# Kernel optimization log

Hardware: AMD Instinct MI355X
Metric: run time of the kernel (lower is better)

## Reference

```python
import jax, jax.numpy as jnp
import numpy as np

FRAME_NUMBER = 1200

def _relgcn(x, W, rows, cols, vals, n_nodes):
    # Multi-relation sparse GCN: sum_r A_r @ (x @ W_r), then tanh.
    out = jnp.zeros((n_nodes, W.shape[-1]), dtype=x.dtype)
    for r in range(W.shape[0]):  # fixed small set of relations (5)
        xl = x @ W[r]                              # [N, D]
        msgs = vals[r][:, None] * xl[cols[r]]      # [E, D] gather
        out = out + jax.ops.segment_sum(msgs, rows[r], num_segments=n_nodes)
    return jnp.tanh(out)

def setup_inputs() -> dict:
    key = jax.random.key(0)
    ks = jax.random.split(key, 20)
    N, E, R, D, B, C = 11201, 100000, 5, 512, 32, 16
    s = lambda k, sh, sc=0.05: jax.random.normal(k, sh, dtype=jnp.float32) * sc
    return {
        "target_span": jax.random.normal(ks[0], (B, 4 * 512), dtype=jnp.float32),
        "frame_emb": s(ks[1], (FRAME_NUMBER + 1, D), 1.0),
        "role_emb": s(ks[2], (10001, D), 1.0),
        "rel_W0": s(ks[3], (R, D, D)),
        "rel_W1": s(ks[4], (R, D, D)),
        "span_W1": s(ks[5], (2048, 2048)),
        "span_b1": s(ks[6], (2048,)),
        "span_W2": s(ks[7], (2048, D)),
        "span_b2": s(ks[8], (D,)),
        "fp_W1": s(ks[9], (D, D)),
        "fp_b1": s(ks[10], (D,)),
        "fp_W2": s(ks[11], (D, D)),
        "fp_b2": s(ks[12], (D,)),
        "adj_vals": jax.random.uniform(ks[13], (R, E), dtype=jnp.float32),
        "fe_ids": jax.random.randint(ks[14], (10001,), 0, 10001),
        "adj_rows": jax.random.randint(ks[15], (R, E), 0, N),
        "adj_cols": jax.random.randint(ks[16], (R, E), 0, N),
        "gold_frame_id": jax.random.randint(ks[17], (B,), 0, C),
        "frame_list": jax.random.randint(ks[18], (B, C), 0, FRAME_NUMBER),
    }

def reference(target_span, frame_emb, role_emb, rel_W0, rel_W1,
              span_W1, span_b1, span_W2, span_b2,
              fp_W1, fp_b1, fp_W2, fp_b2, adj_vals,
              fe_ids, adj_rows, adj_cols, gold_frame_id, frame_list):
    B = target_span.shape[0]
    # Embedding lookups (frame_embedding(arange(frame_number)), role_embedding(fe_dict ids))
    all_frame = frame_emb[:FRAME_NUMBER]            # [1200, D]
    all_fe = role_emb[fe_ids]                       # [10001, D]
    x = jnp.concatenate([all_frame, all_fe], axis=0)  # [N, D]
    N = x.shape[0]
    # Two-layer multi-relation GCN over 5 sparse adjacencies
    x = _relgcn(x, rel_W0, adj_rows, adj_cols, adj_vals, N)
    all_embeddings = _relgcn(x, rel_W1, adj_rows, adj_cols, adj_vals, N)  # [N, D]
    # span_fc_layer Mlp: Linear(2048,2048) -> ReLU -> Linear(2048,512) (dropout in eval = identity)
    target_node = jax.nn.relu(target_span @ span_W1 + span_b1) @ span_W2 + span_b2  # [B, D]
    # frame_pred = RoleClassification: Linear -> ReLU -> Linear -> Tanh, then bmm with all node embeddings
    Q = jnp.tanh(jax.nn.relu(target_node @ fp_W1 + fp_b1) @ fp_W2 + fp_b2)          # [B, D]
    pred_frame_weight = jnp.einsum("nd,bd->bn", all_embeddings, Q)[:, :FRAME_NUMBER]  # [B, 1200]
    # gold frame path: one-hot select gold frame id from candidates, gather its node embedding
    gold_frame_label = jnp.take_along_axis(frame_list, gold_frame_id[:, None], axis=1)[:, 0]  # [B]
    frame_node = all_embeddings[gold_frame_label]   # [B, D] (embed_dropout in eval = identity)
    return jnp.concatenate([pred_frame_weight, frame_node], axis=-1)  # [B, 1200+512]
```

## Files before the change

kernel.cpp:

```cpp
#include <hip/hip_runtime.h>
#include <hip/hip_bf16.h>
#include <stdint.h>

typedef unsigned short u16;
typedef __attribute__((ext_vector_type(8))) short short8;
typedef __attribute__((ext_vector_type(4))) float float4v;

#define NNODES 11201
#define MPAD   11264
#define EEDGES 100000
#define RREL   5
#define DDIM   512
#define XLW    2560
#define FRAMES 1200
#define OUTC   1712

__device__ __forceinline__ float bf2f(u16 h) {
    return __uint_as_float(((uint32_t)h) << 16);
}
__device__ __forceinline__ u16 f2bf(float f) {
    uint32_t x = __float_as_uint(f);
    x += 0x7fffu + ((x >> 16) & 1u);
    return (u16)(x >> 16);
}
__device__ __forceinline__ float fast_tanh(float v) {
    v = fminf(fmaxf(v, -10.f), 10.f);
    float ex = __expf(2.f * v);
    return (ex - 1.f) / (ex + 1.f);
}

__global__ void hist_k(const int* __restrict__ rows, int* __restrict__ counts) {
    int tid = blockIdx.x * 256 + threadIdx.x;
    if (tid >= RREL * EEDGES) return;
    int r = tid / EEDGES;
    atomicAdd(&counts[r * NNODES + rows[tid]], 1);
}

__global__ __launch_bounds__(1024) void scan_offsets(const int* __restrict__ counts,
                                                     int* __restrict__ offs,
                                                     int* __restrict__ cursor) {
    const int PER = 11;
    int r = blockIdx.x;
    const int* c = counts + (size_t)r * NNODES;
    int* o = offs + (size_t)r * (NNODES + 1);
    int* cur = cursor + (size_t)r * NNODES;
    __shared__ int wsum[16];
    const int lane = threadIdx.x & 63, wid = threadIdx.x >> 6;
    int base = threadIdx.x * PER;
    int v[PER];
    int s = 0;
    #pragma unroll
    for (int t = 0; t < PER; ++t) {
        int idx = base + t;
        v[t] = (idx < NNODES) ? c[idx] : 0;
        s += v[t];
    }
    int incl = s;
    #pragma unroll
    for (int d = 1; d < 64; d <<= 1) {
        int t = __shfl_up(incl, d, 64);
        if (lane >= d) incl += t;
    }
    if (lane == 63) wsum[wid] = incl;
    __syncthreads();
    if (wid == 0) {
        int wv = (lane < 16) ? wsum[lane] : 0;
        #pragma unroll
        for (int d = 1; d < 16; d <<= 1) {
            int t = __shfl_up(wv, d, 64);
            if (lane >= d) wv += t;
        }
        if (lane < 16) wsum[lane] = wv;
    }
    __syncthreads();
    int run = incl - s + ((wid > 0) ? wsum[wid - 1] : 0);
    #pragma unroll
    for (int t = 0; t < PER; ++t) {
        int idx = base + t;
        if (idx < NNODES) { o[idx] = run; cur[idx] = run; }
        run += v[t];
    }
    if (threadIdx.x == 1023) o[NNODES] = run;
}

__global__ void scatter_k(const int* __restrict__ rows, const int* __restrict__ cols,
                          const float* __restrict__ vals, int* __restrict__ cursor,
                          int* __restrict__ colS, float* __restrict__ valS) {
    int tid = blockIdx.x * 256 + threadIdx.x;
    if (tid >= RREL * EEDGES) return;
    int r = tid / EEDGES;
    int row = rows[tid];
    int pos = atomicAdd(&cursor[r * NNODES + row], 1);
    colS[(size_t)r * EEDGES + pos] = cols[tid];
    valS[(size_t)r * EEDGES + pos] = vals[tid];
}

#define BX_BLOCKS 5601
#define TSP_BLOCKS 256
#define TR_BASE (BX_BLOCKS + TSP_BLOCKS)
__global__ void prep_all(const float* __restrict__ frame_emb,
                         const float* __restrict__ role_emb,
                         const int* __restrict__ fe_ids,
                         const float* __restrict__ ts,
                         const float* __restrict__ w0, const float* __restrict__ w1,
                         const float* __restrict__ s1, const float* __restrict__ s2,
                         const float* __restrict__ f1, const float* __restrict__ f2,
                         u16* __restrict__ x, u16* __restrict__ tsp,
                         u16* __restrict__ w0t, u16* __restrict__ w1t,
                         u16* __restrict__ s1t, u16* __restrict__ s2t,
                         u16* __restrict__ f1t, u16* __restrict__ f2t) {
    int bid = blockIdx.x;
    if (bid < BX_BLOCKS) {
        int t = bid * 256 + threadIdx.x;
        int row = t >> 7, c4 = (t & 127) << 2;
        if (row >= NNODES) return;
        const float* src = (row < FRAMES) ? (frame_emb + (size_t)row * DDIM)
                                          : (role_emb + (size_t)fe_ids[row - FRAMES] * DDIM);
        float4 v = *(const float4*)(src + c4);
        ushort4 o = { f2bf(v.x), f2bf(v.y), f2bf(v.z), f2bf(v.w) };
        *(ushort4*)(x + (size_t)row * DDIM + c4) = o;
        return;
    }
    if (bid < TR_BASE) {
        int t = (bid - BX_BLOCKS) * 256 + threadIdx.x;
        int row = t >> 9, c4 = (t & 511) << 2;
        ushort4 o = {0, 0, 0, 0};
        if (row < 32) {
            float4 v = *(const float4*)(ts + (size_t)row * 2048 + c4);
            o = ushort4{ f2bf(v.x), f2bf(v.y), f2bf(v.z), f2bf(v.w) };
        }
        *(ushort4*)(tsp + (size_t)row * 2048 + c4) = o;
        return;
    }
    int b = bid - TR_BASE;
    const float* src; u16* dst;
    int cols, ldOut, bx, by;
    size_t zcol = 0;
    if (b < 1280) {
        int rel = b >> 8, rem = b & 255;
        src = w0 + (size_t)rel * 262144; dst = w0t;
        cols = 512; ldOut = XLW; zcol = (size_t)rel * 512;
        bx = rem & 15; by = rem >> 4;
    } else if (b < 2560) {
        b -= 1280;
        int rel = b >> 8, rem = b & 255;
        src = w1 + (size_t)rel * 262144; dst = w1t;
        cols = 512; ldOut = XLW; zcol = (size_t)rel * 512;
        bx = rem & 15; by = rem >> 4;
    } else if (b < 6656) {
        b -= 2560;
        src = s1; dst = s1t; cols = 2048; ldOut = 2048;
        bx = b & 63; by = b >> 6;
    } else if (b < 7680) {
        b -= 6656;
        src = s2; dst = s2t; cols = 512; ldOut = 2048;
        bx = b & 15; by = b >> 4;
    } else if (b < 7936) {
        b -= 7680;
        src = f1; dst = f1t; cols = 512; ldOut = 512;
        bx = b & 15; by = b >> 4;
    } else {
        b -= 7936;
        src = f2; dst = f2t; cols = 512; ldOut = 512;
        bx = b & 15; by = b >> 4;
    }
    __shared__ u16 tile[32][33];
    int c0 = bx * 32, r0 = by * 32;
    int tx = threadIdx.x & 31, ty = threadIdx.x >> 5;
    #pragma unroll
    for (int i = 0; i < 4; ++i) {
        int rr = ty + i * 8;
        tile[rr][tx] = f2bf(src[(size_t)(r0 + rr) * cols + c0 + tx]);
    }
    __syncthreads();
    #pragma unroll
    for (int i = 0; i < 4; ++i) {
        int rr = ty + i * 8;
        dst[(size_t)(c0 + rr) * ldOut + zcol + r0 + tx] = tile[tx][rr];
    }
}

template<int EPI, bool FOUT, bool GUARDS>
__global__ __launch_bounds__(256)
void gemm_n64(const u16* __restrict__ A, const u16* __restrict__ Bt,
              void* __restrict__ Cv, int K, int lda, int ldb, int ldc,
              int mGuard, int nGuard)
{
    __shared__ u16 As[2][128 * 32];
    __shared__ u16 Bs[2][64 * 32];
    const int tid = threadIdx.x;
    const int wave = tid >> 6, lane = tid & 63;
    const int m0 = blockIdx.x * 128, n0 = blockIdx.y * 64;
    const int srow = lane >> 2;
    const int skoff = (lane & 3) << 3;
    const int fr = lane & 15, quad = lane >> 4;
    const int wm = (wave & 1) << 6;
    const int wn = (wave >> 1) << 5;
    float4v acc[4][2] = {};

    const u16* Abase = A  + (size_t)(m0 + srow) * lda + skoff;
    const u16* Bbase = Bt + (size_t)(n0 + srow) * ldb + skoff;

    auto stage = [&](int buf, int k0) {
        #pragma unroll
        for (int i = 0; i < 2; ++i) {
            const int rb = (wave + i * 4) << 4;
            __builtin_amdgcn_global_load_lds(
                (const __attribute__((address_space(1))) unsigned int*)(Abase + (size_t)rb * lda + k0),
                (__attribute__((address_space(3))) unsigned int*)(&As[buf][rb * 32]), 16, 0, 0);
        }
        const int rbB = wave << 4;
        __builtin_amdgcn_global_load_lds(
            (const __attribute__((address_space(1))) unsigned int*)(Bbase + (size_t)rbB * ldb + k0),
            (__attribute__((address_space(3))) unsigned int*)(&Bs[buf][rbB * 32]), 16, 0, 0);
    };
    auto compute = [&](int buf) {
        short8 a[4], b[2];
        #pragma unroll
        for (int t = 0; t < 4; ++t)
            a[t] = *(const short8*)(&As[buf][((wm + t * 16 + fr) << 5) + (quad << 3)]);
        #pragma unroll
        for (int t = 0; t < 2; ++t)
            b[t] = *(const short8*)(&Bs[buf][((wn + t * 16 + fr) << 5) + (quad << 3)]);
        #pragma unroll
        for (int i = 0; i < 4; ++i)
            #pragma unroll
            for (int j = 0; j < 2; ++j)
                acc[i][j] = __builtin_amdgcn_mfma_f32_16x16x32_bf16(a[i], b[j], acc[i][j], 0, 0, 0);
    };

    stage(0, 0);
    __syncthreads();
    int cur = 0;
    for (int k0 = 32; k0 < K; k0 += 32) {
        stage(cur ^ 1, k0);
        compute(cur);
        __syncthreads();
        cur ^= 1;
    }
    compute(cur);

    #pragma unroll
    for (int i = 0; i < 4; ++i) {
        #pragma unroll
        for (int j = 0; j < 2; ++j) {
            const int n = n0 + wn + j * 16 + fr;
            #pragma unroll
            for (int rg = 0; rg < 4; ++rg) {
                const int m = m0 + wm + i * 16 + (quad << 2) + rg;
                if (GUARDS && (m >= mGuard || n >= nGuard)) continue;
                float v = acc[i][j][rg];
                if (EPI == 4) v = fast_tanh(v);
                if (FOUT) ((float*)Cv)[(size_t)m * ldc + n] = v;
                else      ((u16*)Cv)[(size_t)m * ldc + n] = f2bf(v);
            }
        }
    }
}

__global__ __launch_bounds__(256)
void gemm_sk(const u16* __restrict__ A, const u16* __restrict__ Bt,
             float* __restrict__ Cf, int Kc, int lda, int ldb, int ldc)
{
    __shared__ u16 As[2][128 * 32];
    __shared__ u16 Bs[2][128 * 32];
    const int tid = threadIdx.x;
    const int wave = tid >> 6, lane = tid & 63;
    const int m0 = blockIdx.y * 128, n0 = blockIdx.x * 128;
    const int kb = blockIdx.z * Kc;
    const int srow = lane >> 2;
    const int skoff = (lane & 3) << 3;
    const int fr = lane & 15, quad = lane >> 4;
    const int wm = (wave & 1) << 6, wn = (wave >> 1) << 6;
    float4v acc[4][4] = {};

    const u16* Abase = A  + (size_t)(m0 + srow) * lda + skoff;
    const u16* Bbase = Bt + (size_t)(n0 + srow) * ldb + skoff;

    auto stage = [&](int buf, int k0) {
        #pragma unroll
        for (int i = 0; i < 2; ++i) {
            const int rb = (wave + i * 4) << 4;
            __builtin_amdgcn_global_load_lds(
                (const __attribute__((address_space(1))) unsigned int*)(Abase + (size_t)rb * lda + k0),
                (__attribute__((address_space(3))) unsigned int*)(&As[buf][rb * 32]), 16, 0, 0);
            __builtin_amdgcn_global_load_lds(
                (const __attribute__((address_space(1))) unsigned int*)(Bbase + (size_t)rb * ldb + k0),
                (__attribute__((address_space(3))) unsigned int*)(&Bs[buf][rb * 32]), 16, 0, 0);
        }
    };
    auto compute = [&](int buf) {
        short8 a[4], b[4];
        #pragma unroll
        for (int t = 0; t < 4; ++t)
            a[t] = *(const short8*)(&As[buf][((wm + t * 16 + fr) << 5) + (quad << 3)]);
        #pragma unroll
        for (int t = 0; t < 4; ++t)
            b[t] = *(const short8*)(&Bs[buf][((wn + t * 16 + fr) << 5) + (quad << 3)]);
        #pragma unroll
        for (int i = 0; i < 4; ++i)
            #pragma unroll
            for (int j = 0; j < 4; ++j)
                acc[i][j] = __builtin_amdgcn_mfma_f32_16x16x32_bf16(a[i], b[j], acc[i][j], 0, 0, 0);
    };

    stage(0, kb);
    __syncthreads();
    int cur = 0;
    for (int k0 = kb + 32; k0 < kb + Kc; k0 += 32) {
        stage(cur ^ 1, k0);
        compute(cur);
        __syncthreads();
        cur ^= 1;
    }
    compute(cur);

    #pragma unroll
    for (int i = 0; i < 4; ++i)
        #pragma unroll
        for (int j = 0; j < 4; ++j) {
            const int n = n0 + wn + j * 16 + fr;
            #pragma unroll
            for (int rg = 0; rg < 4; ++rg) {
                const int m = m0 + wm + i * 16 + (quad << 2) + rg;
                atomicAdd(&Cf[(size_t)m * ldc + n], acc[i][j][rg]);
            }
        }
}

template<int ACT, bool HASB>
__global__ void sk_ep(const float* __restrict__ Cf, const float* __restrict__ bias,
                      u16* __restrict__ outp, int Ncols, int total4) {
    int t = blockIdx.x * 256 + threadIdx.x;
    if (t >= total4) return;
    int i = t << 2;
    float4 v = *(const float4*)(Cf + i);
    if (HASB) {
        int col = i & (Ncols - 1);
        v.x += bias[col]; v.y += bias[col + 1]; v.z += bias[col + 2]; v.w += bias[col + 3];
    }
    if (ACT == 1) { v.x = fmaxf(v.x, 0.f); v.y = fmaxf(v.y, 0.f);
                    v.z = fmaxf(v.z, 0.f); v.w = fmaxf(v.w, 0.f); }
    if (ACT == 3) { v.x = fast_tanh(v.x); v.y = fast_tanh(v.y);
                    v.z = fast_tanh(v.z); v.w = fast_tanh(v.w); }
    ushort4 o = { f2bf(v.x), f2bf(v.y), f2bf(v.z), f2bf(v.w) };
    *(ushort4*)(outp + i) = o;
}

__device__ __forceinline__ void fma8(float* acc, uint4 u, float val) {
    acc[0] = fmaf(val, __uint_as_float(u.x << 16), acc[0]);
    acc[1] = fmaf(val, __uint_as_float(u.x & 0xffff0000u), acc[1]);
    acc[2] = fmaf(val, __uint_as_float(u.y << 16), acc[2]);
    acc[3] = fmaf(val, __uint_as_float(u.y & 0xffff0000u), acc[3]);
    acc[4] = fmaf(val, __uint_as_float(u.z << 16), acc[4]);
    acc[5] = fmaf(val, __uint_as_float(u.z & 0xffff0000u), acc[5]);
    acc[6] = fmaf(val, __uint_as_float(u.w << 16), acc[6]);
    acc[7] = fmaf(val, __uint_as_float(u.w & 0xffff0000u), acc[7]);
}

__global__ __launch_bounds__(256)
void spmm_agg(const u16* __restrict__ x, const int* __restrict__ offs,
              const int* __restrict__ colS, const float* __restrict__ valS,
              u16* __restrict__ agg)
{
    const int wave = threadIdx.x >> 6, lane = threadIdx.x & 63;
    const int n = blockIdx.x * 4 + wave;
    const int r = blockIdx.y;
    if (n >= NNODES) return;
    const u16* xr = x + (lane << 3);
    int s = offs[r * (NNODES + 1) + n];
    const int e = offs[r * (NNODES + 1) + n + 1];
    const int*   cp = colS + (size_t)r * EEDGES;
    const float* vp = valS + (size_t)r * EEDGES;
    float acc[8] = {0.f, 0.f, 0.f, 0.f, 0.f, 0.f, 0.f, 0.f};
    while (s < e) {
        int m = e - s; if (m > 8) m = 8;
        int   ct[8]; float vt[8]; uint4 u[8];
        #pragma unroll
        for (int t = 0; t < 8; ++t)
            if (t < m) { ct[t] = cp[s + t]; vt[t] = vp[s + t]; }
        #pragma unroll
        for (int t = 0; t < 8; ++t)
            if (t < m) u[t] = *(const uint4*)(xr + (size_t)ct[t] * DDIM);
        #pragma unroll
        for (int t = 0; t < 8; ++t)
            if (t < m) fma8(acc, u[t], vt[t]);
        s += 8;
    }
    uint4 o;
    o.x = (uint32_t)f2bf(acc[0]) | ((uint32_t)f2bf(acc[1]) << 16);
    o.y = (uint32_t)f2bf(acc[2]) | ((uint32_t)f2bf(acc[3]) << 16);
    o.z = (uint32_t)f2bf(acc[4]) | ((uint32_t)f2bf(acc[5]) << 16);
    o.w = (uint32_t)f2bf(acc[6]) | ((uint32_t)f2bf(acc[7]) << 16);
    *(uint4*)(agg + (size_t)n * XLW + (r << 9) + (lane << 3)) = o;
}

__global__ void frame_gather(const u16* __restrict__ emb, const int* __restrict__ frame_list,
                             const int* __restrict__ gold, float* __restrict__ out) {
    int t = blockIdx.x * 256 + threadIdx.x;
    if (t >= 32 * 64) return;
    int b = t >> 6, lane = t & 63;
    int label = frame_list[b * 16 + gold[b]];
    const u16* src = emb + (size_t)label * DDIM + (lane << 3);
    float* dst = out + (size_t)b * OUTC + FRAMES + (lane << 3);
    float4 o0 = { bf2f(src[0]), bf2f(src[1]), bf2f(src[2]), bf2f(src[3]) };
    float4 o1 = { bf2f(src[4]), bf2f(src[5]), bf2f(src[6]), bf2f(src[7]) };
    *(float4*)(dst) = o0;
    *(float4*)(dst + 4) = o1;
}

extern "C" void kernel_launch(void* const* d_in, const int* in_sizes, int n_in,
                              void* d_out, int out_size, void* d_ws, size_t ws_size,
                              hipStream_t stream) {
    const float* target_span = (const float*)d_in[0];
    const float* frame_emb   = (const float*)d_in[1];
    const float* role_emb    = (const float*)d_in[2];
    const float* rel_W0      = (const float*)d_in[3];
    const float* rel_W1      = (const float*)d_in[4];
    const float* span_W1     = (const float*)d_in[5];
    const float* span_b1     = (const float*)d_in[6];
    const float* span_W2     = (const float*)d_in[7];
    const float* span_b2     = (const float*)d_in[8];
    const float* fp_W1       = (const float*)d_in[9];
    const float* fp_b1       = (const float*)d_in[10];
    const float* fp_W2       = (const float*)d_in[11];
    const float* fp_b2       = (const float*)d_in[12];
    const float* adj_vals    = (const float*)d_in[13];
    const int* fe_ids      = (const int*)d_in[14];
    const int* adj_rows    = (const int*)d_in[15];
    const int* adj_cols    = (const int*)d_in[16];
    const int* gold_id     = (const int*)d_in[17];
    const int* frame_list  = (const int*)d_in[18];
    float* out = (float*)d_out;

    char* ws = (char*)d_ws;
    size_t off = 0;
    auto take = [&](size_t bytes) -> char* {
        char* p = ws + off;
        off = (off + bytes + 255) & ~(size_t)255;
        return p;
    };
    u16* x      = (u16*)take((size_t)MPAD * DDIM * 2);
    u16* agg    = (u16*)take((size_t)MPAD * XLW * 2);
    u16* w0t    = (u16*)take((size_t)512 * XLW * 2);
    u16* w1t    = (u16*)take((size_t)512 * XLW * 2);
    u16* s1t    = (u16*)take((size_t)2048 * 2048 * 2);
    u16* s2t    = (u16*)take((size_t)512 * 2048 * 2);
    u16* f1t    = (u16*)take((size_t)512 * 512 * 2);
    u16* f2t    = (u16*)take((size_t)512 * 512 * 2);
    int* counts = (int*)take((size_t)RREL * NNODES * 4);
    int* offs   = (int*)take((size_t)RREL * (NNODES + 1) * 4);
    int* cursor = (int*)take((size_t)RREL * NNODES * 4);
    int* colS   = (int*)take((size_t)RREL * EEDGES * 4);
    float* valS = (float*)take((size_t)RREL * EEDGES * 4);
    u16* tsp    = (u16*)take((size_t)128 * 2048 * 2);
    u16* h1     = (u16*)take((size_t)128 * 2048 * 2);
    u16* tn     = (u16*)take((size_t)128 * 512 * 2);
    u16* h2     = (u16*)take((size_t)128 * 512 * 2);
    u16* Qb     = (u16*)take((size_t)128 * 512 * 2);
    float* CfAll = (float*)take((size_t)(128 * 2048 + 3 * 128 * 512) * 4);
    float* Cf1 = CfAll;
    float* Cf2 = Cf1 + 128 * 2048;
    float* Cf3 = Cf2 + 128 * 512;
    float* Cf4 = Cf3 + 128 * 512;

    hipMemsetAsync(counts, 0, (size_t)RREL * NNODES * 4, stream);
    hipMemsetAsync(CfAll, 0, (size_t)(128 * 2048 + 3 * 128 * 512) * 4, stream);

    hist_k<<<(RREL * EEDGES + 255) / 256, 256, 0, stream>>>(adj_rows, counts);
    scan_offsets<<<RREL, 1024, 0, stream>>>(counts, offs, cursor);
    scatter_k<<<(RREL * EEDGES + 255) / 256, 256, 0, stream>>>(adj_rows, adj_cols, adj_vals,
                                                               cursor, colS, valS);
    prep_all<<<TR_BASE + 8192, 256, 0, stream>>>(frame_emb, role_emb, fe_ids, target_span,
                                                 rel_W0, rel_W1, span_W1, span_W2, fp_W1, fp_W2,
                                                 x, tsp, w0t, w1t, s1t, s2t, f1t, f2t);

    spmm_agg<<<dim3((NNODES + 3) / 4, RREL), 256, 0, stream>>>(x, offs, colS, valS, agg);
    gemm_n64<4, false, true><<<dim3(MPAD / 128, 8), 256, 0, stream>>>(
        agg, w0t, x, XLW, XLW, XLW, 512, NNODES, 512);
    spmm_agg<<<dim3((NNODES + 3) / 4, RREL), 256, 0, stream>>>(x, offs, colS, valS, agg);
    gemm_n64<4, false, true><<<dim3(MPAD / 128, 8), 256, 0, stream>>>(
        agg, w1t, x, XLW, XLW, XLW, 512, NNODES, 512);

    gemm_sk<<<dim3(16, 1, 8), 256, 0, stream>>>(tsp, s1t, Cf1, 256, 2048, 2048, 2048);
    sk_ep<1, true><<<(128 * 2048 / 4 + 255) / 256, 256, 0, stream>>>(Cf1, span_b1, h1, 2048, 128 * 2048 / 4);
    gemm_sk<<<dim3(4, 1, 8), 256, 0, stream>>>(h1, s2t, Cf2, 256, 2048, 2048, 512);
    sk_ep<0, true><<<(128 * 512 / 4 + 255) / 256, 256, 0, stream>>>(Cf2, span_b2, tn, 512, 128 * 512 / 4);
    gemm_sk<<<dim3(4, 1, 4), 256, 0, stream>>>(tn, f1t, Cf3, 128, 512, 512, 512);
    sk_ep<1, true><<<(128 * 512 / 4 + 255) / 256, 256, 0, stream>>>(Cf3, fp_b1, h2, 512, 128 * 512 / 4);
    gemm_sk<<<dim3(4, 1, 4), 256, 0, stream>>>(h2, f2t, Cf4, 128, 512, 512, 512);
    sk_ep<3, true><<<(128 * 512 / 4 + 255) / 256, 256, 0, stream>>>(Cf4, fp_b2, Qb, 512, 128 * 512 / 4);

    gemm_n64<0, true, true><<<dim3(1, 19), 256, 0, stream>>>(
        Qb, x, out, 512, 512, 512, OUTC, 32, FRAMES);
    frame_gather<<<8, 256, 0, stream>>>(x, frame_list, gold_id, out);
}
```

Before: 485.9 us.

## Replace LDS-staged GEMM with direct register-load MFMA GEMM and merge memsets

The 128x64 tiled GEMM no longer stages A and B through double-buffered shared memory. Each wave now loads its MFMA fragments straight from global memory into registers and runs an unrolled K loop with no __syncthreads. This removes the LDS traffic and barrier overhead, but loses cross-wave reuse of the B tile: all four waves reload the same B rows and depend on cache hits. Separately, the workspace layout is reordered so one memset zeroes both the counts and split-K accumulator buffers, which also zeroes the buffers that lie between them.

Measured after the change: 707.6 us. 45.6% more time.

```diff
diff --git a/kernel.cpp b/kernel.cpp
--- a/kernel.cpp
+++ b/kernel.cpp
@@ -182,72 +182,45 @@
 
 template<int EPI, bool FOUT, bool GUARDS>
 __global__ __launch_bounds__(256)
-void gemm_n64(const u16* __restrict__ A, const u16* __restrict__ Bt,
+void gemm_reg(const u16* __restrict__ A, const u16* __restrict__ Bt,
               void* __restrict__ Cv, int K, int lda, int ldb, int ldc,
               int mGuard, int nGuard)
 {
-    __shared__ u16 As[2][128 * 32];
-    __shared__ u16 Bs[2][64 * 32];
-    const int tid = threadIdx.x;
-    const int wave = tid >> 6, lane = tid & 63;
+    const int lane = threadIdx.x & 63, wave = threadIdx.x >> 6;
+    const int fr = lane & 15, quad = lane >> 4;
     const int m0 = blockIdx.x * 128, n0 = blockIdx.y * 64;
-    const int srow = lane >> 2;
-    const int skoff = (lane & 3) << 3;
-    const int fr = lane & 15, quad = lane >> 4;
-    const int wm = (wave & 1) << 6;
-    const int wn = (wave >> 1) << 5;
-    float4v acc[4][2] = {};
-
-    const u16* Abase = A  + (size_t)(m0 + srow) * lda + skoff;
-    const u16* Bbase = Bt + (size_t)(n0 + srow) * ldb + skoff;
-
-    auto stage = [&](int buf, int k0) {
-        #pragma unroll
-        for (int i = 0; i < 2; ++i) {
-            const int rb = (wave + i * 4) << 4;
-            __builtin_amdgcn_global_load_lds(
-                (const __attribute__((address_space(1))) unsigned int*)(Abase + (size_t)rb * lda + k0),
-                (__attribute__((address_space(3))) unsigned int*)(&As[buf][rb * 32]), 16, 0, 0);
-        }
-        const int rbB = wave << 4;
-        __builtin_amdgcn_global_load_lds(
-            (const __attribute__((address_space(1))) unsigned int*)(Bbase + (size_t)rbB * ldb + k0),
-            (__attribute__((address_space(3))) unsigned int*)(&Bs[buf][rbB * 32]), 16, 0, 0);
-    };
-    auto compute = [&](int buf) {
-        short8 a[4], b[2];
-        #pragma unroll
-        for (int t = 0; t < 4; ++t)
-            a[t] = *(const short8*)(&As[buf][((wm + t * 16 + fr) << 5) + (quad << 3)]);
-        #pragma unroll
-        for (int t = 0; t < 2; ++t)
-            b[t] = *(const short8*)(&Bs[buf][((wn + t * 16 + fr) << 5) + (quad << 3)]);
-        #pragma unroll
-        for (int i = 0; i < 4; ++i)
-            #pragma unroll
-            for (int j = 0; j < 2; ++j)
-                acc[i][j] = __builtin_amdgcn_mfma_f32_16x16x32_bf16(a[i], b[j], acc[i][j], 0, 0, 0);
-    };
-
-    stage(0, 0);
-    __syncthreads();
-    int cur = 0;
-    for (int k0 = 32; k0 < K; k0 += 32) {
-        stage(cur ^ 1, k0);
-        compute(cur);
-        __syncthreads();
-        cur ^= 1;
-    }
-    compute(cur);
-
-    #pragma unroll
-    for (int i = 0; i < 4; ++i) {
-        #pragma unroll
-        for (int j = 0; j < 2; ++j) {
-            const int n = n0 + wn + j * 16 + fr;
+    const u16* Ap = A  + (size_t)(m0 + (wave << 5) + fr) * lda + (quad << 3);
+    const u16* Bp = Bt + (size_t)(n0 + fr) * ldb + (quad << 3);
+    const size_t lda16 = (size_t)lda * 16;
+    const size_t ldb16 = (size_t)ldb * 16;
+    float4v acc[2][4] = {};
+
+    #pragma unroll 4
+    for (int k0 = 0; k0 < K; k0 += 32) {
+        short8 a0 = *(const short8*)(Ap + k0);
+        short8 a1 = *(const short8*)(Ap + lda16 + k0);
+        short8 b0 = *(const short8*)(Bp + k0);
+        short8 b1 = *(const short8*)(Bp + ldb16 + k0);
+        short8 b2 = *(const short8*)(Bp + 2 * ldb16 + k0);
+        short8 b3 = *(const short8*)(Bp + 3 * ldb16 + k0);
+        acc[0][0] = __builtin_amdgcn_mfma_f32_16x16x32_bf16(a0, b0, acc[0][0], 0, 0, 0);
+        acc[0][1] = __builtin_amdgcn_mfma_f32_16x16x32_bf16(a0, b1, acc[0][1], 0, 0, 0);
+        acc[0][2] = __builtin_amdgcn_mfma_f32_16x16x32_bf16(a0, b2, acc[0][2], 0, 0, 0);
+        acc[0][3] = __builtin_amdgcn_mfma_f32_16x16x32_bf16(a0, b3, acc[0][3], 0, 0, 0);
+        acc[1][0] = __builtin_amdgcn_mfma_f32_16x16x32_bf16(a1, b0, acc[1][0], 0, 0, 0);
+        acc[1][1] = __builtin_amdgcn_mfma_f32_16x16x32_bf16(a1, b1, acc[1][1], 0, 0, 0);
+        acc[1][2] = __builtin_amdgcn_mfma_f32_16x16x32_bf16(a1, b2, acc[1][2], 0, 0, 0);
+        acc[1][3] = __builtin_amdgcn_mfma_f32_16x16x32_bf16(a1, b3, acc[1][3], 0, 0, 0);
+    }
+
+    #pragma unroll
+    for (int i = 0; i < 2; ++i) {
+        #pragma unroll
+        for (int j = 0; j < 4; ++j) {
+            const int n = n0 + j * 16 + fr;
             #pragma unroll
             for (int rg = 0; rg < 4; ++rg) {
-                const int m = m0 + wm + i * 16 + (quad << 2) + rg;
+                const int m = m0 + (wave << 5) + i * 16 + (quad << 2) + rg;
                 if (GUARDS && (m >= mGuard || n >= nGuard)) continue;
                 float v = acc[i][j][rg];
                 if (EPI == 4) v = fast_tanh(v);
@@ -449,6 +422,7 @@
     u16* f1t    = (u16*)take((size_t)512 * 512 * 2);
     u16* f2t    = (u16*)take((size_t)512 * 512 * 2);
     int* counts = (int*)take((size_t)RREL * NNODES * 4);
+    float* CfAll = (float*)take((size_t)(128 * 2048 + 3 * 128 * 512) * 4);
     int* offs   = (int*)take((size_t)RREL * (NNODES + 1) * 4);
     int* cursor = (int*)take((size_t)RREL * NNODES * 4);
     int* colS   = (int*)take((size_t)RREL * EEDGES * 4);
@@ -458,14 +432,13 @@
     u16* tn     = (u16*)take((size_t)128 * 512 * 2);
     u16* h2     = (u16*)take((size_t)128 * 512 * 2);
     u16* Qb     = (u16*)take((size_t)128 * 512 * 2);
-    float* CfAll = (float*)take((size_t)(128 * 2048 + 3 * 128 * 512) * 4);
     float* Cf1 = CfAll;
     float* Cf2 = Cf1 + 128 * 2048;
     float* Cf3 = Cf2 + 128 * 512;
     float* Cf4 = Cf3 + 128 * 512;
 
-    hipMemsetAsync(counts, 0, (size_t)RREL * NNODES * 4, stream);
-    hipMemsetAsync(CfAll, 0, (size_t)(128 * 2048 + 3 * 128 * 512) * 4, stream);
+    size_t zlen = (char*)(CfAll + 128 * 2048 + 3 * 128 * 512) - (char*)counts;
+    hipMemsetAsync(counts, 0, zlen, stream);
 
     hist_k<<<(RREL * EEDGES + 255) / 256, 256, 0, stream>>>(adj_rows, counts);
     scan_offsets<<<RREL, 1024, 0, stream>>>(counts, offs, cursor);
@@ -476,10 +449,10 @@
                                                  x, tsp, w0t, w1t, s1t, s2t, f1t, f2t);
 
     spmm_agg<<<dim3((NNODES + 3) / 4, RREL), 256, 0, stream>>>(x, offs, colS, valS, agg);
-    gemm_n64<4, false, true><<<dim3(MPAD / 128, 8), 256, 0, stream>>>(
+    gemm_reg<4, false, true><<<dim3(MPAD / 128, 8), 256, 0, stream>>>(
         agg, w0t, x, XLW, XLW, XLW, 512, NNODES, 512);
     spmm_agg<<<dim3((NNODES + 3) / 4, RREL), 256, 0, stream>>>(x, offs, colS, valS, agg);
-    gemm_n64<4, false, true><<<dim3(MPAD / 128, 8), 256, 0, stream>>>(
+    gemm_reg<4, false, true><<<dim3(MPAD / 128, 8), 256, 0, stream>>>(
         agg, w1t, x, XLW, XLW, XLW, 512, NNODES, 512);
 
     gemm_sk<<<dim3(16, 1, 8), 256, 0, stream>>>(tsp, s1t, Cf1, 256, 2048, 2048, 2048);
@@ -491,7 +464,7 @@
     gemm_sk<<<dim3(4, 1, 4), 256, 0, stream>>>(h2, f2t, Cf4, 128, 512, 512, 512);
     sk_ep<3, true><<<(128 * 512 / 4 + 255) / 256, 256, 0, stream>>>(Cf4, fp_b2, Qb, 512, 128 * 512 / 4);
 
-    gemm_n64<0, true, true><<<dim3(1, 19), 256, 0, stream>>>(
+    gemm_reg<0, true, true><<<dim3(1, 19), 256, 0, stream>>>(
         Qb, x, out, 512, 512, 512, OUTC, 32, FRAMES);
     frame_gather<<<8, 256, 0, stream>>>(x, frame_list, gold_id, out);
 }
```

## Co-schedule small MLP GEMMs inside GCN kernels and merge launches

Applied to the files above, without the earlier changes.

The span and frame-prediction MLP GEMMs (previously split-K with atomics plus separate epilogue kernels and a memset) now run as extra blocks appended to the SpMM and big GEMM launches. They compute full K per block with fused bias and activation. The histogram is folded into the prep kernel, and the prediction GEMM and gold-frame gather share one launch. The big GEMM now stages K=64 per iteration. The aim is fewer launches, no atomics or memset, and letting the small MLP work overlap the GCN stages. The cost is that each MLP block runs a long serial K loop on only 16-64 blocks, which could become the tail of each kernel.

Result: faster. 457.0 us (-5.9%).

```diff
diff --git a/kernel.cpp b/kernel.cpp
--- a/kernel.cpp
+++ b/kernel.cpp
@@ -15,6 +15,9 @@
 #define FRAMES 1200
 #define OUTC   1712
 
+#define AS1 __attribute__((address_space(1)))
+#define AS3 __attribute__((address_space(3)))
+
 __device__ __forceinline__ float bf2f(u16 h) {
     return __uint_as_float(((uint32_t)h) << 16);
 }
@@ -28,12 +31,8 @@
     float ex = __expf(2.f * v);
     return (ex - 1.f) / (ex + 1.f);
 }
-
-__global__ void hist_k(const int* __restrict__ rows, int* __restrict__ counts) {
-    int tid = blockIdx.x * 256 + threadIdx.x;
-    if (tid >= RREL * EEDGES) return;
-    int r = tid / EEDGES;
-    atomicAdd(&counts[r * NNODES + rows[tid]], 1);
+__device__ __forceinline__ void gl_lds(const u16* g, u16* l) {
+    __builtin_amdgcn_global_load_lds((const AS1 unsigned int*)g, (AS3 unsigned int*)l, 16, 0, 0);
 }
 
 __global__ __launch_bounds__(1024) void scan_offsets(const int* __restrict__ counts,
@@ -98,18 +97,29 @@
 #define BX_BLOCKS 5601
 #define TSP_BLOCKS 256
 #define TR_BASE (BX_BLOCKS + TSP_BLOCKS)
-__global__ void prep_all(const float* __restrict__ frame_emb,
-                         const float* __restrict__ role_emb,
-                         const int* __restrict__ fe_ids,
-                         const float* __restrict__ ts,
-                         const float* __restrict__ w0, const float* __restrict__ w1,
-                         const float* __restrict__ s1, const float* __restrict__ s2,
-                         const float* __restrict__ f1, const float* __restrict__ f2,
-                         u16* __restrict__ x, u16* __restrict__ tsp,
-                         u16* __restrict__ w0t, u16* __restrict__ w1t,
-                         u16* __restrict__ s1t, u16* __restrict__ s2t,
-                         u16* __restrict__ f1t, u16* __restrict__ f2t) {
+#define HIST_BASE (TR_BASE + 8192)
+#define HIST_BLKS 1954
+__global__ void prep_hist(const float* __restrict__ frame_emb,
+                          const float* __restrict__ role_emb,
+                          const int* __restrict__ fe_ids,
+                          const float* __restrict__ ts,
+                          const float* __restrict__ w0, const float* __restrict__ w1,
+                          const float* __restrict__ s1, const float* __restrict__ s2,
+                          const float* __restrict__ f1, const float* __restrict__ f2,
+                          u16* __restrict__ x, u16* __restrict__ tsp,
+                          u16* __restrict__ w0t, u16* __restrict__ w1t,
+                          u16* __restrict__ s1t, u16* __restrict__ s2t,
+                          u16* __restrict__ f1t, u16* __restrict__ f2t,
+                          const int* __restrict__ adj_rows, int* __restrict__ counts) {
     int bid = blockIdx.x;
+    if (bid >= HIST_BASE) {
+        int t = (bid - HIST_BASE) * 256 + threadIdx.x;
+        if (t < RREL * EEDGES) {
+            int r = t / EEDGES;
+            atomicAdd(&counts[r * NNODES + adj_rows[t]], 1);
+        }
+        return;
+    }
     if (bid < BX_BLOCKS) {
         int t = bid * 256 + threadIdx.x;
         int row = t >> 7, c4 = (t & 127) << 2;
@@ -180,173 +190,60 @@
     }
 }
 
-template<int EPI, bool FOUT, bool GUARDS>
-__global__ __launch_bounds__(256)
-void gemm_n64(const u16* __restrict__ A, const u16* __restrict__ Bt,
-              void* __restrict__ Cv, int K, int lda, int ldb, int ldc,
-              int mGuard, int nGuard)
+__device__ __forceinline__ void mlp_gemm(int bid, u16* lds,
+    const u16* __restrict__ A, const u16* __restrict__ Bt, u16* __restrict__ C,
+    const float* __restrict__ bias, int K, int lda, int ldb, int ldc, int act)
 {
-    __shared__ u16 As[2][128 * 32];
-    __shared__ u16 Bs[2][64 * 32];
     const int tid = threadIdx.x;
     const int wave = tid >> 6, lane = tid & 63;
-    const int m0 = blockIdx.x * 128, n0 = blockIdx.y * 64;
-    const int srow = lane >> 2;
-    const int skoff = (lane & 3) << 3;
     const int fr = lane & 15, quad = lane >> 4;
-    const int wm = (wave & 1) << 6;
-    const int wn = (wave >> 1) << 5;
-    float4v acc[4][2] = {};
-
-    const u16* Abase = A  + (size_t)(m0 + srow) * lda + skoff;
-    const u16* Bbase = Bt + (size_t)(n0 + srow) * ldb + skoff;
-
-    auto stage = [&](int buf, int k0) {
-        #pragma unroll
-        for (int i = 0; i < 2; ++i) {
-            const int rb = (wave + i * 4) << 4;
-            __builtin_amdgcn_global_load_lds(
-                (const __attribute__((address_space(1))) unsigned int*)(Abase + (size_t)rb * lda + k0),
-                (__attribute__((address_space(3))) unsigned int*)(&As[buf][rb * 32]), 16, 0, 0);
-        }
-        const int rbB = wave << 4;
-        __builtin_amdgcn_global_load_lds(
-            (const __attribute__((address_space(1))) unsigned int*)(Bbase + (size_t)rbB * ldb + k0),
-            (__attribute__((address_space(3))) unsigned int*)(&Bs[buf][rbB * 32]), 16, 0, 0);
-    };
-    auto compute = [&](int buf) {
-        short8 a[4], b[2];
-        #pragma unroll
-        for (int t = 0; t < 4; ++t)
-            a[t] = *(const short8*)(&As[buf][((wm + t * 16 + fr) << 5) + (quad << 3)]);
-        #pragma unroll
-        for (int t = 0; t < 2; ++t)
-            b[t] = *(const short8*)(&Bs[buf][((wn + t * 16 + fr) << 5) + (quad << 3)]);
-        #pragma unroll
-        for (int i = 0; i < 4; ++i)
-            #pragma unroll
-            for (int j = 0; j < 2; ++j)
-                acc[i][j] = __builtin_amdgcn_mfma_f32_16x16x32_bf16(a[i], b[j], acc[i][j], 0, 0, 0);
-    };
-
+    const int m0 = (bid & 1) << 6, n0 = (bid >> 1) << 6;
+    const int srow = tid >> 2, sk = (tid & 3) << 3;
+    const u16* Ab = A + (size_t)(m0 + srow) * lda + sk;
+    const u16* Bb = Bt + (size_t)(n0 + srow) * ldb + sk;
+    const int lo = srow * 32 + sk;
+    float4v acc[4] = {};
+
+    auto stage = [&](int b, int k0) {
+        gl_lds(Ab + k0, lds + b * 4096 + lo);
+        gl_lds(Bb + k0, lds + b * 4096 + 2048 + lo);
+    };
+    auto comp = [&](int b) {
+        const u16* As = lds + b * 4096;
+        const u16* Bs = As + 2048;
+        short8 bb = *(const short8*)(Bs + (((wave << 4) + fr) << 5) + (quad << 3));
+        #pragma unroll
+        for (int t = 0; t < 4; ++t) {
+            short8 aa = *(const short8*)(As + ((t * 16 + fr) << 5) + (quad << 3));
+            acc[t] = __builtin_amdgcn_mfma_f32_16x16x32_bf16(aa, bb, acc[t], 0, 0, 0);
+        }
+    };
     stage(0, 0);
     __syncthreads();
-    int cur = 0;
+    int buf = 0;
     for (int k0 = 32; k0 < K; k0 += 32) {
-        stage(cur ^ 1, k0);
-        compute(cur);
+        stage(buf ^ 1, k0);
+        comp(buf);
         __syncthreads();
-        cur ^= 1;
-    }
-    compute(cur);
-
-    #pragma unroll
-    for (int i = 0; i < 4; ++i) {
-        #pragma unroll
-        for (int j = 0; j < 2; ++j) {
-            const int n = n0 + wn + j * 16 + fr;
-            #pragma unroll
-            for (int rg = 0; rg < 4; ++rg) {
-                const int m = m0 + wm + i * 16 + (quad << 2) + rg;
-                if (GUARDS && (m >= mGuard || n >= nGuard)) continue;
-                float v = acc[i][j][rg];
-                if (EPI == 4) v = fast_tanh(v);
-                if (FOUT) ((float*)Cv)[(size_t)m * ldc + n] = v;
-                else      ((u16*)Cv)[(size_t)m * ldc + n] = f2bf(v);
-            }
-        }
-    }
-}
-
-__global__ __launch_bounds__(256)
-void gemm_sk(const u16* __restrict__ A, const u16* __restrict__ Bt,
-             float* __restrict__ Cf, int Kc, int lda, int ldb, int ldc)
-{
-    __shared__ u16 As[2][128 * 32];
-    __shared__ u16 Bs[2][128 * 32];
-    const int tid = threadIdx.x;
-    const int wave = tid >> 6, lane = tid & 63;
-    const int m0 = blockIdx.y * 128, n0 = blockIdx.x * 128;
-    const int kb = blockIdx.z * Kc;
-    const int srow = lane >> 2;
-    const int skoff = (lane & 3) << 3;
-    const int fr = lane & 15, quad = lane >> 4;
-    const int wm = (wave & 1) << 6, wn = (wave >> 1) << 6;
-    float4v acc[4][4] = {};
-
-    const u16* Abase = A  + (size_t)(m0 + srow) * lda + skoff;
-    const u16* Bbase = Bt + (size_t)(n0 + srow) * ldb + skoff;
-
-    auto stage = [&](int buf, int k0) {
-        #pragma unroll
-        for (int i = 0; i < 2; ++i) {
-            const int rb = (wave + i * 4) << 4;
-            __builtin_amdgcn_global_load_lds(
-                (const __attribute__((address_space(1))) unsigned int*)(Abase + (size_t)rb * lda + k0),
-                (__attribute__((address_space(3))) unsigned int*)(&As[buf][rb * 32]), 16, 0, 0);
-            __builtin_amdgcn_global_load_lds(
-                (const __attribute__((address_space(1))) unsigned int*)(Bbase + (size_t)rb * ldb + k0),
-                (__attribute__((address_space(3))) unsigned int*)(&Bs[buf][rb * 32]), 16, 0, 0);
-        }
-    };
-    auto compute = [&](int buf) {
-        short8 a[4], b[4];
-        #pragma unroll
-        for (int t = 0; t < 4; ++t)
-            a[t] = *(const short8*)(&As[buf][((wm + t * 16 + fr) << 5) + (quad << 3)]);
-        #pragma unroll
-        for (int t = 0; t < 4; ++t)
-            b[t] = *(const short8*)(&Bs[buf][((wn + t * 16 + fr) << 5) + (quad << 3)]);
-        #pragma unroll
-        for (int i = 0; i < 4; ++i)
-            #pragma unroll
-            for (int j = 0; j < 4; ++j)
-                acc[i][j] = __builtin_amdgcn_mfma_f32_16x16x32_bf16(a[i], b[j], acc[i][j], 0, 0, 0);
-    };
-
-    stage(0, kb);
-    __syncthreads();
-    int cur = 0;
-    for (int k0 = kb + 32; k0 < kb + Kc; k0 += 32) {
-        stage(cur ^ 1, k0);
-        compute(cur);
-        __syncthreads();
-        cur ^= 1;
-    }
-    compute(cur);
-
-    #pragma unroll
-    for (int i = 0; i < 4; ++i)
-        #pragma unroll
-        for (int j = 0; j < 4; ++j) {
-            const int n = n0 + wn + j * 16 + fr;
-            #pragma unroll
-            for (int rg = 0; rg < 4; ++rg) {
-                const int m = m0 + wm + i * 16 + (quad << 2) + rg;
-                atomicAdd(&Cf[(size_t)m * ldc + n], acc[i][j][rg]);
-            }
-        }
-}
-
-template<int ACT, bool HASB>
-__global__ void sk_ep(const float* __restrict__ Cf, const float* __restrict__ bias,
-                      u16* __restrict__ outp, int Ncols, int total4) {
-    int t = blockIdx.x * 256 + threadIdx.x;
-    if (t >= total4) return;
-    int i = t << 2;
-    float4 v = *(const float4*)(Cf + i);
-    if (HASB) {
-        int col = i & (Ncols - 1);
-        v.x += bias[col]; v.y += bias[col + 1]; v.z += bias[col + 2]; v.w += bias[col + 3];
-    }
-    if (ACT == 1) { v.x = fmaxf(v.x, 0.f); v.y = fmaxf(v.y, 0.f);
-                    v.z = fmaxf(v.z, 0.f); v.w = fmaxf(v.w, 0.f); }
-    if (ACT == 3) { v.x = fast_tanh(v.x); v.y = fast_tanh(v.y);
-                    v.z = fast_tanh(v.z); v.w = fast_tanh(v.w); }
-    ushort4 o = { f2bf(v.x), f2bf(v.y), f2bf(v.z), f2bf(v.w) };
-    *(ushort4*)(outp + i) = o;
-}
-
+        buf ^= 1;
+    }
+    comp(buf);
+
+    const int n = n0 + (wave << 4) + fr;
+    float bv = bias[n];
+    #pragma unroll
+    for (int t = 0; t < 4; ++t)
+        #pragma unroll
+        for (int rg = 0; rg < 4; ++rg) {
+            int m = m0 + t * 16 + (quad << 2) + rg;
+            float v = acc[t][rg] + bv;
+            if (act == 1) v = fmaxf(v, 0.f);
+            if (act == 2) v = fast_tanh(v);
+            C[(size_t)m * ldc + n] = f2bf(v);
+        }
+}
+
+#define SPMM_BLKS 14005
 __device__ __forceinline__ void fma8(float* acc, uint4 u, float val) {
     acc[0] = fmaf(val, __uint_as_float(u.x << 16), acc[0]);
     acc[1] = fmaf(val, __uint_as_float(u.x & 0xffff0000u), acc[1]);
@@ -359,13 +256,22 @@
 }
 
 __global__ __launch_bounds__(256)
-void spmm_agg(const u16* __restrict__ x, const int* __restrict__ offs,
+void spmm_mlp(const u16* __restrict__ x, const int* __restrict__ offs,
               const int* __restrict__ colS, const float* __restrict__ valS,
-              u16* __restrict__ agg)
+              u16* __restrict__ agg,
+              const u16* __restrict__ mA, const u16* __restrict__ mBt,
+              u16* __restrict__ mC, const float* __restrict__ mBias,
+              int mK, int mLda, int mLdb, int mLdc, int mAct)
 {
+    __shared__ u16 lds[8192];
+    const int bid = blockIdx.x;
+    if (bid >= SPMM_BLKS) {
+        mlp_gemm(bid - SPMM_BLKS, lds, mA, mBt, mC, mBias, mK, mLda, mLdb, mLdc, mAct);
+        return;
+    }
     const int wave = threadIdx.x >> 6, lane = threadIdx.x & 63;
-    const int n = blockIdx.x * 4 + wave;
-    const int r = blockIdx.y;
+    const int r = bid / 2801;
+    const int n = (bid - r * 2801) * 4 + wave;
     if (n >= NNODES) return;
     const u16* xr = x + (lane << 3);
     int s = offs[r * (NNODES + 1) + n];
@@ -395,18 +301,150 @@
     *(uint4*)(agg + (size_t)n * XLW + (r << 9) + (lane << 3)) = o;
 }
 
-__global__ void frame_gather(const u16* __restrict__ emb, const int* __restrict__ frame_list,
-                             const int* __restrict__ gold, float* __restrict__ out) {
-    int t = blockIdx.x * 256 + threadIdx.x;
-    if (t >= 32 * 64) return;
-    int b = t >> 6, lane = t & 63;
-    int label = frame_list[b * 16 + gold[b]];
-    const u16* src = emb + (size_t)label * DDIM + (lane << 3);
-    float* dst = out + (size_t)b * OUTC + FRAMES + (lane << 3);
-    float4 o0 = { bf2f(src[0]), bf2f(src[1]), bf2f(src[2]), bf2f(src[3]) };
-    float4 o1 = { bf2f(src[4]), bf2f(src[5]), bf2f(src[6]), bf2f(src[7]) };
-    *(float4*)(dst) = o0;
-    *(float4*)(dst + 4) = o1;
+#define GBLK 704
+__global__ __launch_bounds__(256)
+void gemm_mlp(const u16* __restrict__ A, const u16* __restrict__ Bt,
+              u16* __restrict__ C, int mGuard,
+              const u16* __restrict__ mA, const u16* __restrict__ mBt,
+              u16* __restrict__ mC, const float* __restrict__ mBias,
+              int mK, int mLda, int mLdb, int mLdc, int mAct)
+{
+    __shared__ u16 lds[2][12288];
+    const int bid = blockIdx.x;
+    const int tid = threadIdx.x;
+    if (bid >= GBLK) {
+        mlp_gemm(bid - GBLK, &lds[0][0], mA, mBt, mC, mBias, mK, mLda, mLdb, mLdc, mAct);
+        return;
+    }
+    const int wave = tid >> 6, lane = tid & 63;
+    const int fr = lane & 15, quad = lane >> 4;
+    const int bm = bid % 88, bn = bid / 88;
+    const int m0 = bm << 7, n0 = bn << 6;
+    const int srow = tid >> 3, sk = (tid & 7) << 3;
+    const u16* Ab = A + (size_t)(m0 + srow) * XLW + sk;
+    const u16* Bb = Bt + (size_t)(n0 + srow) * XLW + sk;
+    const int wm = (wave & 1) << 6, wn = (wave >> 1) << 5;
+    const int lo = (srow << 6) + sk;
+    float4v acc[4][2] = {};
+
+    auto stage = [&](int b, int k0) {
+        u16* As = &lds[b][0];
+        u16* Bs = &lds[b][8192];
+        #pragma unroll
+        for (int c = 0; c < 4; ++c)
+            gl_lds(Ab + (size_t)(c * 32) * XLW + k0, As + c * 2048 + lo);
+        #pragma unroll
+        for (int c = 0; c < 2; ++c)
+            gl_lds(Bb + (size_t)(c * 32) * XLW + k0, Bs + c * 2048 + lo);
+    };
+    auto comp = [&](int b) {
+        const u16* As = &lds[b][0];
+        const u16* Bs = &lds[b][8192];
+        #pragma unroll
+        for (int s = 0; s < 2; ++s) {
+            short8 a[4], bb[2];
+            #pragma unroll
+            for (int t = 0; t < 4; ++t)
+                a[t] = *(const short8*)(As + ((wm + t * 16 + fr) << 6) + (s << 5) + (quad << 3));
+            #pragma unroll
+            for (int t = 0; t < 2; ++t)
+                bb[t] = *(const short8*)(Bs + ((wn + t * 16 + fr) << 6) + (s << 5) + (quad << 3));
+            #pragma unroll
+            for (int i = 0; i < 4; ++i)
+                #pragma unroll
+                for (int j = 0; j < 2; ++j)
+                    acc[i][j] = __builtin_amdgcn_mfma_f32_16x16x32_bf16(a[i], bb[j], acc[i][j], 0, 0, 0);
+        }
+    };
+
+    stage(0, 0);
+    __syncthreads();
+    int buf = 0;
+    for (int k0 = 64; k0 < XLW; k0 += 64) {
+        stage(buf ^ 1, k0);
+        comp(buf);
+        __syncthreads();
+        buf ^= 1;
+    }
+    comp(buf);
+
+    #pragma unroll
+    for (int i = 0; i < 4; ++i)
+        #pragma unroll
+        for (int j = 0; j < 2; ++j) {
+            const int n = n0 + wn + j * 16 + fr;
+            #pragma unroll
+            for (int rg = 0; rg < 4; ++rg) {
+                const int m = m0 + wm + i * 16 + (quad << 2) + rg;
+                if (m < mGuard)
+                    C[(size_t)m * 512 + n] = f2bf(fast_tanh(acc[i][j][rg]));
+            }
+        }
+}
+
+__global__ __launch_bounds__(256)
+void pred_fg(const u16* __restrict__ Q, const u16* __restrict__ E,
+             float* __restrict__ out,
+             const int* __restrict__ frame_list, const int* __restrict__ gold)
+{
+    __shared__ u16 lds[8192];
+    const int bid = blockIdx.x;
+    const int tid = threadIdx.x;
+    if (bid >= 19) {
+        int t = (bid - 19) * 256 + tid;
+        if (t >= 32 * 64) return;
+        int b = t >> 6, lane = t & 63;
+        int label = frame_list[b * 16 + gold[b]];
+        const u16* src = E + (size_t)label * DDIM + (lane << 3);
+        float* dst = out + (size_t)b * OUTC + FRAMES + (lane << 3);
+        float4 o0 = { bf2f(src[0]), bf2f(src[1]), bf2f(src[2]), bf2f(src[3]) };
+        float4 o1 = { bf2f(src[4]), bf2f(src[5]), bf2f(src[6]), bf2f(src[7]) };
+        *(float4*)(dst) = o0;
+        *(float4*)(dst + 4) = o1;
+        return;
+    }
+    const int wave = tid >> 6, lane = tid & 63;
+    const int fr = lane & 15, quad = lane >> 4;
+    const int n0 = bid << 6;
+    const int srow = tid >> 2, sk = (tid & 3) << 3;
+    const u16* Ab = Q + (size_t)srow * 512 + sk;
+    const u16* Bb = E + (size_t)(n0 + srow) * 512 + sk;
+    const int lo = (srow << 5) + sk;
+    float4v acc[4] = {};
+    auto stage = [&](int b, int k0) {
+        gl_lds(Ab + k0, lds + b * 4096 + lo);
+        gl_lds(Bb + k0, lds + b * 4096 + 2048 + lo);
+    };
+    auto comp = [&](int b) {
+        const u16* As = lds + b * 4096;
+        const u16* Bs = As + 2048;
+        short8 bb = *(const short8*)(Bs + (((wave << 4) + fr) << 5) + (quad << 3));
+        #pragma unroll
+        for (int t = 0; t < 4; ++t) {
+            short8 aa = *(const short8*)(As + ((t * 16 + fr) << 5) + (quad << 3));
+            acc[t] = __builtin_amdgcn_mfma_f32_16x16x32_bf16(aa, bb, acc[t], 0, 0, 0);
+        }
+    };
+    stage(0, 0);
+    __syncthreads();
+    int buf = 0;
+    for (int k0 = 32; k0 < 512; k0 += 32) {
+        stage(buf ^ 1, k0);
+        comp(buf);
+        __syncthreads();
+        buf ^= 1;
+    }
+    comp(buf);
+    const int n = n0 + (wave << 4) + fr;
+    if (n >= FRAMES) return;
+    #pragma unroll
+    for (int t = 0; t < 4; ++t)
+        #pragma unroll
+        for (int rg = 0; rg < 4; ++rg) {
+            int m = t * 16 + (quad << 2) + rg;
+            if (m < 32)
+                out[(size_t)m * OUTC + n] = acc[t][rg];
+        }
 }
 
 extern "C" void kernel_launch(void* const* d_in, const int* in_sizes, int n_in,
@@ -458,40 +496,23 @@
     u16* tn     = (u16*)take((size_t)128 * 512 * 2);
     u16* h2     = (u16*)take((size_t)128 * 512 * 2);
     u16* Qb     = (u16*)take((size_t)128 * 512 * 2);
-    float* CfAll = (float*)take((size_t)(128 * 2048 + 3 * 128 * 512) * 4);
-    float* Cf1 = CfAll;
-    float* Cf2 = Cf1 + 128 * 2048;
-    float* Cf3 = Cf2 + 128 * 512;
-    float* Cf4 = Cf3 + 128 * 512;
 
     hipMemsetAsync(counts, 0, (size_t)RREL * NNODES * 4, stream);
-    hipMemsetAsync(CfAll, 0, (size_t)(128 * 2048 + 3 * 128 * 512) * 4, stream);
-
-    hist_k<<<(RREL * EEDGES + 255) / 256, 256, 0, stream>>>(adj_rows, counts);
+
+    prep_hist<<<HIST_BASE + HIST_BLKS, 256, 0, stream>>>(
+        frame_emb, role_emb, fe_ids, target_span,
+        rel_W0, rel_W1, span_W1, span_W2, fp_W1, fp_W2,
+        x, tsp, w0t, w1t, s1t, s2t, f1t, f2t, adj_rows, counts);
     scan_offsets<<<RREL, 1024, 0, stream>>>(counts, offs, cursor);
     scatter_k<<<(RREL * EEDGES + 255) / 256, 256, 0, stream>>>(adj_rows, adj_cols, adj_vals,
                                                                cursor, colS, valS);
-    prep_all<<<TR_BASE + 8192, 256, 0, stream>>>(frame_emb, role_emb, fe_ids, target_span,
-                                                 rel_W0, rel_W1, span_W1, span_W2, fp_W1, fp_W2,
-                                                 x, tsp, w0t, w1t, s1t, s2t, f1t, f2t);
-
-    spmm_agg<<<dim3((NNODES + 3) / 4, RREL), 256, 0, stream>>>(x, offs, colS, valS, agg);
-    gemm_n64<4, false, true><<<dim3(MPAD / 128, 8), 256, 0, stream>>>(
-        agg, w0t, x, XLW, XLW, XLW, 512, NNODES, 512);
-    spmm_agg<<<dim3((NNODES + 3) / 4, RREL), 256, 0, stream>>>(x, offs, colS, valS, agg);
-    gemm_n64<4, false, true><<<dim3(MPAD / 128, 8), 256, 0, stream>>>(
-        agg, w1t, x, XLW, XLW, XLW, 512, NNODES, 512);
-
-    gemm_sk<<<dim3(16, 1, 8), 256, 0, stream>>>(tsp, s1t, Cf1, 256, 2048, 2048, 2048);
-    sk_ep<1, true><<<(128 * 2048 / 4 + 255) / 256, 256, 0, stream>>>(Cf1, span_b1, h1, 2048, 128 * 2048 / 4);
-    gemm_sk<<<dim3(4, 1, 8), 256, 0, stream>>>(h1, s2t, Cf2, 256, 2048, 2048, 512);
-    sk_ep<0, true><<<(128 * 512 / 4 + 255) / 256, 256, 0, stream>>>(Cf2, span_b2, tn, 512, 128 * 512 / 4);
-    gemm_sk<<<dim3(4, 1, 4), 256, 0, stream>>>(tn, f1t, Cf3, 128, 512, 512, 512);
-    sk_ep<1, true><<<(128 * 512 / 4 + 255) / 256, 256, 0, stream>>>(Cf3, fp_b1, h2, 512, 128 * 512 / 4);
-    gemm_sk<<<dim3(4, 1, 4), 256, 0, stream>>>(h2, f2t, Cf4, 128, 512, 512, 512);
-    sk_ep<3, true><<<(128 * 512 / 4 + 255) / 256, 256, 0, stream>>>(Cf4, fp_b2, Qb, 512, 128 * 512 / 4);
-
-    gemm_n64<0, true, true><<<dim3(1, 19), 256, 0, stream>>>(
-        Qb, x, out, 512, 512, 512, OUTC, 32, FRAMES);
-    frame_gather<<<8, 256, 0, stream>>>(x, frame_list, gold_id, out);
-}
+    spmm_mlp<<<SPMM_BLKS + 64, 256, 0, stream>>>(x, offs, colS, valS, agg,
+                                                 tsp, s1t, h1, span_b1, 2048, 2048, 2048, 2048, 1);
+    gemm_mlp<<<GBLK + 16, 256, 0, stream>>>(agg, w0t, x, NNODES,
+                                            h1, s2t, tn, span_b2, 2048, 2048, 2048, 512, 0);
+    spmm_mlp<<<SPMM_BLKS + 16, 256, 0, stream>>>(x, offs, colS, valS, agg,
+                                                 tn, f1t, h2, fp_b1, 512, 512, 512, 512, 1);
+    gemm_mlp<<<GBLK + 16, 256, 0, stream>>>(agg, w1t, x, NNODES,
+                                            h2, f2t, Qb, fp_b2, 512, 512, 512, 512, 2);
+    pred_fg<<<19 + 8, 256, 0, stream>>>(Qb, x, out, frame_list, gold_id);
+}
```
